# Kernel tuning notes

Measured on AMD Instinct MI355X. Metric: run time of the kernel, lower is better.

## Reference

```python
import jax, jax.numpy as jnp
import numpy as np

N_NODES = 50000
N_EDGES = 800000
IN_DIM = 128
HIDDEN = 16
HEADS1 = 8
OUT_DIM = 128
NEG_SLOPE = 0.2
EPS = 1e-16


def gat_conv(x, src, dst, W, att_src, att_dst, bias, heads, out_ch, concat, num_nodes):
    # x: [N, F_in]; W: [F_in, heads*out_ch]; att_*: [heads, out_ch]; bias: [heads*out_ch] or [out_ch]
    h = (x @ W).reshape(num_nodes, heads, out_ch)          # [N, H, C]
    a_src = jnp.einsum('nhc,hc->nh', h, att_src)           # [N, H]
    a_dst = jnp.einsum('nhc,hc->nh', h, att_dst)           # [N, H]
    alpha = a_src[src] + a_dst[dst]                        # [E, H]
    alpha = jax.nn.leaky_relu(alpha, NEG_SLOPE)
    # segment softmax over incoming edges of each dst node
    amax = jax.ops.segment_max(alpha, dst, num_segments=num_nodes)  # [N, H]
    e = jnp.exp(alpha - amax[dst])                         # [E, H]
    denom = jax.ops.segment_sum(e, dst, num_segments=num_nodes)     # [N, H]
    alpha = e / (denom[dst] + EPS)                         # [E, H]
    msg = h[src] * alpha[:, :, None]                       # [E, H, C]
    out = jax.ops.segment_sum(msg, dst, num_segments=num_nodes)     # [N, H, C]
    if concat:
        out = out.reshape(num_nodes, heads * out_ch)
    else:
        out = out.mean(axis=1)
    return out + bias


def setup_inputs() -> dict:
    key = jax.random.key(0)
    ks = jax.random.split(key, 12)
    x = jax.random.normal(ks[0], (N_NODES, IN_DIM), dtype=jnp.float32)
    edge_index = jax.random.randint(ks[1], (2, N_EDGES), 0, N_NODES, dtype=jnp.int32)
    s1 = 1.0 / np.sqrt(IN_DIM)
    s2 = 1.0 / np.sqrt(HIDDEN * HEADS1)
    W1 = jax.random.normal(ks[2], (IN_DIM, HEADS1 * HIDDEN), dtype=jnp.float32) * s1
    att_src1 = jax.random.normal(ks[3], (HEADS1, HIDDEN), dtype=jnp.float32) * s1
    att_dst1 = jax.random.normal(ks[4], (HEADS1, HIDDEN), dtype=jnp.float32) * s1
    bias1 = jnp.zeros((HEADS1 * HIDDEN,), dtype=jnp.float32)
    W2 = jax.random.normal(ks[5], (HEADS1 * HIDDEN, OUT_DIM), dtype=jnp.float32) * s2
    att_src2 = jax.random.normal(ks[6], (1, OUT_DIM), dtype=jnp.float32) * s2
    att_dst2 = jax.random.normal(ks[7], (1, OUT_DIM), dtype=jnp.float32) * s2
    bias2 = jnp.zeros((OUT_DIM,), dtype=jnp.float32)
    return {"x": x, "edge_index": edge_index,
            "W1": W1, "att_src1": att_src1, "att_dst1": att_dst1, "bias1": bias1,
            "W2": W2, "att_src2": att_src2, "att_dst2": att_dst2, "bias2": bias2}


def reference(x, edge_index, W1, att_src1, att_dst1, bias1, W2, att_src2, att_dst2, bias2):
    # eval mode: F.dropout and attention dropout are identity
    src, dst = edge_index[0], edge_index[1]
    h = gat_conv(x, src, dst, W1, att_src1, att_dst1, bias1,
                 HEADS1, HIDDEN, True, N_NODES)            # [N, HEADS1*HIDDEN]
    h = jax.nn.elu(h)
    out = gat_conv(h, src, dst, W2, att_src2, att_dst2, bias2,
                   1, OUT_DIM, False, N_NODES)             # [N, OUT_DIM]
    return out
```

## Files before the change

### kernel.cpp

```cpp
#include <hip/hip_runtime.h>

#define N_NODES 50000
#define N_EDGES 800000
#define CAP 64
#define NBUCK 196
#define NODES_PAD 50176
#define BBLK 256
#define EPB 3125
#define LOG2E 1.4426950408889634f

typedef unsigned int uint;
typedef unsigned short ushort;
typedef __attribute__((ext_vector_type(2))) float f32x2;
typedef __attribute__((ext_vector_type(4))) float f32x4;
typedef __attribute__((ext_vector_type(8))) short s16x8;

__device__ __forceinline__ f32x2 pk_add(f32x2 a, f32x2 b) {
    f32x2 d;
    asm("v_pk_add_f32 %0, %1, %2" : "=v"(d) : "v"(a), "v"(b));
    return d;
}
__device__ __forceinline__ f32x2 pk_mul(f32x2 a, f32x2 b) {
    f32x2 d;
    asm("v_pk_mul_f32 %0, %1, %2" : "=v"(d) : "v"(a), "v"(b));
    return d;
}
__device__ __forceinline__ f32x2 pk_fma(f32x2 a, f32x2 b, f32x2 c) {
    f32x2 d;
    asm("v_pk_fma_f32 %0, %1, %2, %3" : "=v"(d) : "v"(a), "v"(b), "v"(c));
    return d;
}

__device__ __forceinline__ ushort f2bf(float f) {
    uint u = __float_as_uint(f);
    u = (u + 0x7fffu + ((u >> 16) & 1u)) >> 16;
    return (ushort)u;
}
__device__ __forceinline__ float bf_lo(uint u) { return __uint_as_float(u << 16); }
__device__ __forceinline__ float bf_hi(uint u) { return __uint_as_float(u & 0xffff0000u); }

__global__ __launch_bounds__(256) void bin_count_kernel(
    const int* __restrict__ dstv, uint* __restrict__ counts)
{
    __shared__ uint hist[NBUCK];
    int tid = threadIdx.x, b = blockIdx.x;
    for (int k = tid; k < NBUCK; k += 256) hist[k] = 0;
    __syncthreads();
    int e0 = b * EPB;
    for (int i = tid; i < EPB; i += 256)
        atomicAdd(&hist[((uint)dstv[e0 + i]) >> 8], 1u);
    __syncthreads();
    for (int k = tid; k < NBUCK; k += 256) counts[k * BBLK + b] = hist[k];
}

__global__ __launch_bounds__(256) void scan1_kernel(
    const uint* __restrict__ counts, uint* __restrict__ ofs, uint* __restrict__ bsum)
{
    __shared__ uint wtot[4];
    int tid = threadIdx.x, k = blockIdx.x;
    int lane = tid & 63, wid = tid >> 6;
    uint v = counts[k * 256 + tid];
    uint inc = v;
    #pragma unroll
    for (int o = 1; o < 64; o <<= 1) {
        uint t = __shfl_up(inc, o);
        if (lane >= o) inc += t;
    }
    if (lane == 63) wtot[wid] = inc;
    __syncthreads();
    uint woff = 0;
    for (int w = 0; w < wid; w++) woff += wtot[w];
    uint excl = woff + inc - v;
    ofs[k * 256 + tid] = excl;
    if (tid == 255) bsum[k] = excl + v;
}

__global__ __launch_bounds__(64) void scan2_kernel(
    const uint* __restrict__ bsum, uint* __restrict__ bbase)
{
    int lane = threadIdx.x;
    int base = lane * 4;
    uint v[4];
    #pragma unroll
    for (int j = 0; j < 4; j++) v[j] = (base + j < NBUCK) ? bsum[base + j] : 0u;
    uint s = v[0] + v[1] + v[2] + v[3];
    uint inc = s;
    #pragma unroll
    for (int o = 1; o < 64; o <<= 1) {
        uint t = __shfl_up(inc, o);
        if (lane >= o) inc += t;
    }
    uint run = inc - s;
    #pragma unroll
    for (int j = 0; j < 4; j++) {
        if (base + j < NBUCK) { bbase[base + j] = run; run += v[j]; }
    }
}

__global__ __launch_bounds__(256) void bin_scatter_kernel(
    const int* __restrict__ srcv, const int* __restrict__ dstv,
    const uint* __restrict__ ofs, const uint* __restrict__ bbase,
    uint* __restrict__ binned)
{
    __shared__ uint cur[NBUCK];
    int tid = threadIdx.x, b = blockIdx.x;
    for (int k = tid; k < NBUCK; k += 256) cur[k] = ofs[k * BBLK + b] + bbase[k];
    __syncthreads();
    int e0 = b * EPB;
    for (int i = tid; i < EPB; i += 256) {
        int d = dstv[e0 + i], s = srcv[e0 + i];
        uint k = ((uint)d) >> 8;
        uint pos = atomicAdd(&cur[k], 1u);
        binned[pos] = (((uint)d & 255u) << 16) | (uint)s;
    }
}

__global__ __launch_bounds__(256) void build_kernel(
    const uint* __restrict__ binned, const uint* __restrict__ ofs,
    const uint* __restrict__ bbase,
    int* __restrict__ deg, ushort* __restrict__ list)
{
    __shared__ uint ldeg[256];
    __shared__ ushort llist[256 * CAP];
    int tid = threadIdx.x, k = blockIdx.x;
    ldeg[tid] = 0;
    __syncthreads();
    uint start = ofs[k * 256] + bbase[k];
    uint end = (k == NBUCK - 1) ? N_EDGES : (ofs[(k + 1) * 256] + bbase[k + 1]);
    for (uint i = start + tid; i < end; i += 256) {
        uint p = binned[i];
        uint nl = (p >> 16) & 255u;
        uint slot = atomicAdd(&ldeg[nl], 1u);
        if (slot < CAP) llist[(nl << 6) + slot] = (ushort)(p & 0xFFFFu);
    }
    __syncthreads();
    int node0 = k << 8;
    deg[node0 + tid] = (int)ldeg[tid];
    uint4* d4 = (uint4*)(list + (size_t)node0 * CAP);
    const uint4* s4 = (const uint4*)llist;
    for (int i = tid; i < 256 * CAP * 2 / 16; i += 256) d4[i] = s4[i];
}

__global__ __launch_bounds__(256) void prep_kernel(
    const float* __restrict__ W1, const float* __restrict__ as1, const float* __restrict__ ad1,
    const float* __restrict__ W2, const float* __restrict__ as2, const float* __restrict__ ad2,
    float* __restrict__ WS1, float* __restrict__ WS2)
{
    int idx = blockIdx.x * 256 + threadIdx.x;
    if (idx < 2048) {
        int k = idx >> 4, j = idx & 15;
        const float* att = (j < 8) ? as1 : ad1;
        int head = j & 7;
        float s = 0.f;
        #pragma unroll
        for (int c = 0; c < 16; c++)
            s += W1[k * 128 + head * 16 + c] * att[head * 16 + c];
        WS1[idx] = s * LOG2E;
    } else if (idx < 4096) {
        int idx2 = idx - 2048;
        int k = idx2 >> 4, j = idx2 & 15;
        float s = 0.f;
        if (j < 2) {
            const float* att = j ? ad2 : as2;
            for (int c = 0; c < 128; c++) s += W2[k * 128 + c] * att[c];
        }
        WS2[idx2] = s * LOG2E;
    }
}

template <int HEADS, bool ABF16>
__global__ __launch_bounds__(512) void gemm_mfma_kernel(
    const void* __restrict__ Av, const float* __restrict__ W,
    const float* __restrict__ WS,
    ushort* __restrict__ h16, float* __restrict__ a_src, float* __restrict__ a_dst,
    int nrows)
{
    __shared__ ushort Bf[2304 * 8];
    int tid = threadIdx.x;
    for (int idx = tid; idx < 2304; idx += 512) {
        int t = idx >> 8;
        int rem = idx & 255;
        int kt = rem >> 6, L = rem & 63;
        int col = L & 15;
        int kb = ((L >> 4) << 3) + (kt << 5);
        ushort tmp[8];
        if (t < 8) {
            #pragma unroll
            for (int j = 0; j < 8; j++)
                tmp[j] = f2bf(W[(size_t)(kb + j) * 128 + (t << 4) + col]);
        } else {
            #pragma unroll
            for (int j = 0; j < 8; j++)
                tmp[j] = f2bf(WS[(kb + j) * 16 + col]);
        }
        uint p0 = (uint)tmp[0] | ((uint)tmp[1] << 16);
        uint p1 = (uint)tmp[2] | ((uint)tmp[3] << 16);
        uint p2 = (uint)tmp[4] | ((uint)tmp[5] << 16);
        uint p3 = (uint)tmp[6] | ((uint)tmp[7] << 16);
        *(uint4*)&Bf[idx * 8] = make_uint4(p0, p1, p2, p3);
    }
    __syncthreads();

    int lane = tid & 63;
    int wv = tid >> 6;
    int row0 = (blockIdx.x * 8 + wv) * 16;
    if (row0 >= nrows) return;

    int m = lane & 15, kg = lane >> 4;
    s16x8 afrag[4];
    if (ABF16) {
        const ushort* arow = (const ushort*)Av + (size_t)(row0 + m) * 128 + (kg << 3);
        #pragma unroll
        for (int kt = 0; kt < 4; kt++)
            afrag[kt] = *(const s16x8*)(arow + (kt << 5));
    } else {
        const float* arow = (const float*)Av + (size_t)(row0 + m) * 128 + (kg << 3);
        #pragma unroll
        for (int kt = 0; kt < 4; kt++) {
            float4 f0 = *(const float4*)(arow + (kt << 5));
            float4 f1 = *(const float4*)(arow + (kt << 5) + 4);
            union { s16x8 v; ushort us[8]; } uu;
            uu.us[0] = f2bf(f0.x); uu.us[1] = f2bf(f0.y);
            uu.us[2] = f2bf(f0.z); uu.us[3] = f2bf(f0.w);
            uu.us[4] = f2bf(f1.x); uu.us[5] = f2bf(f1.y);
            uu.us[6] = f2bf(f1.z); uu.us[7] = f2bf(f1.w);
            afrag[kt] = uu.v;
        }
    }

    f32x4 acc[9];
    #pragma unroll
    for (int t = 0; t < 9; t++) acc[t] = (f32x4){0.f, 0.f, 0.f, 0.f};
    #pragma unroll
    for (int t = 0; t < 9; t++) {
        #pragma unroll
        for (int kt = 0; kt < 4; kt++) {
            s16x8 b = *(const s16x8*)&Bf[(((t << 2) + kt) * 64 + lane) * 8];
            acc[t] = __builtin_amdgcn_mfma_f32_16x16x32_bf16(afrag[kt], b, acc[t], 0, 0, 0);
        }
    }

    int colw = lane & 15;
    int rbase = row0 + ((lane >> 4) << 2);
    #pragma unroll
    for (int t = 0; t < 8; t++) {
        #pragma unroll
        for (int r = 0; r < 4; r++)
            h16[(size_t)(rbase + r) * 128 + (t << 4) + colw] = f2bf(acc[t][r]);
    }
    #pragma unroll
    for (int r = 0; r < 4; r++) {
        float v = acc[8][r];
        int row = rbase + r;
        if (HEADS == 8) {
            if (colw < 8) a_src[row * 8 + colw] = v;
            else          a_dst[row * 8 + (colw - 8)] = v;
        } else {
            if (colw == 0)      a_src[row] = v;
            else if (colw == 1) a_dst[row] = v;
        }
    }
}

template <int HEADS, bool ELU, bool OUT16>
__global__ __launch_bounds__(256) void agg_kernel(
    const ushort* __restrict__ h16, const ushort* __restrict__ list,
    const int* __restrict__ deg,
    const float* __restrict__ a_src, const float* __restrict__ a_dst,
    const float* __restrict__ bias, void* __restrict__ outv)
{
    __shared__ float w_lds[4][HEADS][65];
    __shared__ int s_lds[4][64];
    __shared__ float sh_l[4][8];
    int lane = threadIdx.x & 63;
    int wv = threadIdx.x >> 6;
    int n = blockIdx.x * 4 + wv;
    int d = min(deg[n], CAP);
    bool valid = lane < d;
    int s = valid ? (int)list[n * CAP + lane] : 0;
    s_lds[wv][lane] = s << 8;

    if (HEADS == 8) {
        float4 u0 = *(const float4*)&a_src[s * 8];
        float4 u1 = *(const float4*)&a_src[s * 8 + 4];
        float4 v0 = *(const float4*)&a_dst[n * 8];
        float4 v1 = *(const float4*)&a_dst[n * 8 + 4];
        float al[8] = {u0.x + v0.x, u0.y + v0.y, u0.z + v0.z, u0.w + v0.w,
                       u1.x + v1.x, u1.y + v1.y, u1.z + v1.z, u1.w + v1.w};
        float eh[8];
        #pragma unroll
        for (int hh = 0; hh < 8; hh++) {
            float a = fmaxf(al[hh], 0.2f * al[hh]);
            eh[hh] = valid ? exp2f(a) : 0.f;
            w_lds[wv][hh][lane] = eh[hh];
        }
        f32x2 s01 = {eh[0], eh[1]}, s23 = {eh[2], eh[3]};
        f32x2 s45 = {eh[4], eh[5]}, s67 = {eh[6], eh[7]};
        auto lvl = [&](int mm) {
            f32x2 t;
            t.x = __shfl_xor(s01.x, mm); t.y = __shfl_xor(s01.y, mm); s01 = pk_add(s01, t);
            t.x = __shfl_xor(s23.x, mm); t.y = __shfl_xor(s23.y, mm); s23 = pk_add(s23, t);
            t.x = __shfl_xor(s45.x, mm); t.y = __shfl_xor(s45.y, mm); s45 = pk_add(s45, t);
            t.x = __shfl_xor(s67.x, mm); t.y = __shfl_xor(s67.y, mm); s67 = pk_add(s67, t);
        };
        lvl(1); lvl(2); lvl(4); lvl(8);
        if (d > 16) lvl(16);
        if (d > 32) lvl(32);
        if (lane == 0) {
            *(f32x2*)&sh_l[wv][0] = s01; *(f32x2*)&sh_l[wv][2] = s23;
            *(f32x2*)&sh_l[wv][4] = s45; *(f32x2*)&sh_l[wv][6] = s67;
        }
    } else {
        float a = a_src[s] + a_dst[n];
        a = fmaxf(a, 0.2f * a);
        float eh0 = valid ? exp2f(a) : 0.f;
        w_lds[wv][0][lane] = eh0;
        float sh = eh0;
        sh += __shfl_xor(sh, 1); sh += __shfl_xor(sh, 2);
        sh += __shfl_xor(sh, 4); sh += __shfl_xor(sh, 8);
        if (d > 16) sh += __shfl_xor(sh, 16);
        if (d > 32) sh += __shfl_xor(sh, 32);
        if (lane == 0) sh_l[wv][0] = sh;
    }

    int half = lane >> 5;
    int lq = lane & 31;
    int c0 = lq << 2;
    int g = (HEADS == 8) ? (lq >> 2) : 0;
    const char* hp = (const char*)h16 + (c0 << 1);
    f32x2 acc01 = {0.f, 0.f}, acc23 = {0.f, 0.f};
    int d8 = (d + 7) & ~7;
    for (int e0 = 0; e0 < d8; e0 += 8) {
        int soff[4]; float wv4[4]; uint2 u[4];
        #pragma unroll
        for (int r = 0; r < 4; r++) {
            int e = e0 + (r << 1) + half;
            soff[r] = s_lds[wv][e];
            wv4[r] = w_lds[wv][g][e];
        }
        #pragma unroll
        for (int r = 0; r < 4; r++)
            u[r] = *(const uint2*)(hp + soff[r]);
        #pragma unroll
        for (int r = 0; r < 4; r++) {
            f32x2 wp = {wv4[r], wv4[r]};
            f32x2 lo = {bf_lo(u[r].x), bf_hi(u[r].x)};
            f32x2 hi = {bf_lo(u[r].y), bf_hi(u[r].y)};
            acc01 = pk_fma(wp, lo, acc01);
            acc23 = pk_fma(wp, hi, acc23);
        }
    }
    f32x2 t;
    t.x = __shfl_xor(acc01.x, 32); t.y = __shfl_xor(acc01.y, 32); acc01 = pk_add(acc01, t);
    t.x = __shfl_xor(acc23.x, 32); t.y = __shfl_xor(acc23.y, 32); acc23 = pk_add(acc23, t);

    float shv = sh_l[wv][g];
    float r = __builtin_amdgcn_rcpf(shv + 1e-16f);
    f32x2 rr = {r, r};
    acc01 = pk_mul(acc01, rr);
    acc23 = pk_mul(acc23, rr);
    float4 bv = *(const float4*)&bias[c0];
    float o0 = acc01.x + bv.x, o1 = acc01.y + bv.y;
    float o2 = acc23.x + bv.z, o3 = acc23.y + bv.w;
    if (ELU) {
        o0 = o0 > 0.f ? o0 : __expf(o0) - 1.f;
        o1 = o1 > 0.f ? o1 : __expf(o1) - 1.f;
        o2 = o2 > 0.f ? o2 : __expf(o2) - 1.f;
        o3 = o3 > 0.f ? o3 : __expf(o3) - 1.f;
    }
    if (lane < 32) {
        if (OUT16) {
            uint2 pk;
            pk.x = (uint)f2bf(o0) | ((uint)f2bf(o1) << 16);
            pk.y = (uint)f2bf(o2) | ((uint)f2bf(o3) << 16);
            *(uint2*)((ushort*)outv + (size_t)n * 128 + c0) = pk;
        } else {
            *(float4*)((float*)outv + (size_t)n * 128 + c0) = make_float4(o0, o1, o2, o3);
        }
    }
}

extern "C" void kernel_launch(void* const* d_in, const int* in_sizes, int n_in,
                              void* d_out, int out_size, void* d_ws, size_t ws_size,
                              hipStream_t stream)
{
    (void)in_sizes; (void)n_in; (void)out_size; (void)ws_size;
    const float* x   = (const float*)d_in[0];
    const int*   ei  = (const int*)d_in[1];
    const float* W1  = (const float*)d_in[2];
    const float* as1 = (const float*)d_in[3];
    const float* ad1 = (const float*)d_in[4];
    const float* b1  = (const float*)d_in[5];
    const float* W2  = (const float*)d_in[6];
    const float* as2 = (const float*)d_in[7];
    const float* ad2 = (const float*)d_in[8];
    const float* b2  = (const float*)d_in[9];
    float* out = (float*)d_out;
    const int* srcv = ei;
    const int* dstv = ei + N_EDGES;

    char* ws = (char*)d_ws;
    size_t off = 0;
    auto alloc = [&](size_t bytes) {
        void* p = ws + off;
        off += (bytes + 255) & ~(size_t)255;
        return p;
    };
    ushort* h1_16 = (ushort*)alloc((size_t)N_NODES * 128 * 2);
    ushort* h2_16 = (ushort*)alloc((size_t)N_NODES * 128 * 2);
    ushort* h1b   = (ushort*)alloc((size_t)N_NODES * 128 * 2);
    float*  asrc1 = (float*)alloc((size_t)N_NODES * 8 * 4);
    float*  adst1 = (float*)alloc((size_t)N_NODES * 8 * 4);
    float*  asrc2 = (float*)alloc((size_t)N_NODES * 4);
    float*  adst2 = (float*)alloc((size_t)N_NODES * 4);
    int*    degp  = (int*)alloc((size_t)NODES_PAD * 4);
    ushort* list  = (ushort*)alloc((size_t)NODES_PAD * CAP * 2);
    float*  WS1   = (float*)alloc(128 * 16 * 4);
    float*  WS2   = (float*)alloc(128 * 16 * 4);
    uint* binned = (uint*)h1b;
    uint* counts = binned + N_EDGES;
    uint* ofsp   = counts + NODES_PAD;
    uint* bsum   = ofsp + NODES_PAD;
    uint* bbase  = bsum + NBUCK;

    const int NG = (N_NODES + 3) / 4;
    const int GB = (N_NODES / 16 + 7) / 8;

    prep_kernel<<<16, 256, 0, stream>>>(W1, as1, ad1, W2, as2, ad2, WS1, WS2);
    bin_count_kernel<<<BBLK, 256, 0, stream>>>(dstv, counts);
    scan1_kernel<<<NBUCK, 256, 0, stream>>>(counts, ofsp, bsum);
    scan2_kernel<<<1, 64, 0, stream>>>(bsum, bbase);
    bin_scatter_kernel<<<BBLK, 256, 0, stream>>>(srcv, dstv, ofsp, bbase, binned);
    build_kernel<<<NBUCK, 256, 0, stream>>>(binned, ofsp, bbase, degp, list);

    gemm_mfma_kernel<8, false><<<GB, 512, 0, stream>>>(x, W1, WS1, h1_16, asrc1, adst1, N_NODES);
    agg_kernel<8, true, true><<<NG, 256, 0, stream>>>(h1_16, list, degp, asrc1, adst1, b1, h1b);

    gemm_mfma_kernel<1, true><<<GB, 512, 0, stream>>>(h1b, W2, WS2, h2_16, asrc2, adst2, N_NODES);
    agg_kernel<1, false, false><<<NG, 256, 0, stream>>>(h2_16, list, degp, asrc2, adst2, b2, out);
}
```

Baseline: 125.5 us.

## Software-pipeline neighbor feature gathers with double-buffered 16-edge chunks

Result: no change. 124.7 us (-0.7%).

```diff
diff --git a/kernel.cpp b/kernel.cpp
--- a/kernel.cpp
+++ b/kernel.cpp
@@ -280,11 +280,49 @@
     int s = valid ? (int)list[n * CAP + lane] : 0;
     s_lds[wv][lane] = s << 8;
 
+    float4 u0, u1, v0, v1;
+    float a1s = 0.f, a1d = 0.f;
     if (HEADS == 8) {
-        float4 u0 = *(const float4*)&a_src[s * 8];
-        float4 u1 = *(const float4*)&a_src[s * 8 + 4];
-        float4 v0 = *(const float4*)&a_dst[n * 8];
-        float4 v1 = *(const float4*)&a_dst[n * 8 + 4];
+        u0 = *(const float4*)&a_src[s * 8];
+        u1 = *(const float4*)&a_src[s * 8 + 4];
+        v0 = *(const float4*)&a_dst[n * 8];
+        v1 = *(const float4*)&a_dst[n * 8 + 4];
+    } else {
+        a1s = a_src[s]; a1d = a_dst[n];
+    }
+
+    int half = lane >> 5;
+    int lq = lane & 31;
+    int c0 = lq << 2;
+    int g = (HEADS == 8) ? (lq >> 2) : 0;
+    const char* hp = (const char*)h16 + (c0 << 1);
+    int d16 = (d + 15) & ~15;
+
+    uint2 uA[8], uB[8];
+    auto issue = [&](uint2 (&u)[8], int base) {
+        #pragma unroll
+        for (int r = 0; r < 8; r++) {
+            int e = base + (r << 1) + half;
+            u[r] = *(const uint2*)(hp + s_lds[wv][e]);
+        }
+    };
+    f32x2 acc01 = {0.f, 0.f}, acc23 = {0.f, 0.f};
+    auto fmachunk = [&](uint2 (&u)[8], int base) {
+        #pragma unroll
+        for (int r = 0; r < 8; r++) {
+            int e = base + (r << 1) + half;
+            float w = w_lds[wv][g][e];
+            f32x2 wp = {w, w};
+            f32x2 lo = {bf_lo(u[r].x), bf_hi(u[r].x)};
+            f32x2 hi = {bf_lo(u[r].y), bf_hi(u[r].y)};
+            acc01 = pk_fma(wp, lo, acc01);
+            acc23 = pk_fma(wp, hi, acc23);
+        }
+    };
+
+    if (d16 > 0) issue(uA, 0);
+
+    if (HEADS == 8) {
         float al[8] = {u0.x + v0.x, u0.y + v0.y, u0.z + v0.z, u0.w + v0.w,
                        u1.x + v1.x, u1.y + v1.y, u1.z + v1.z, u1.w + v1.w};
         float eh[8];
@@ -311,7 +349,7 @@
             *(f32x2*)&sh_l[wv][4] = s45; *(f32x2*)&sh_l[wv][6] = s67;
         }
     } else {
-        float a = a_src[s] + a_dst[n];
+        float a = a1s + a1d;
         a = fmaxf(a, 0.2f * a);
         float eh0 = valid ? exp2f(a) : 0.f;
         w_lds[wv][0][lane] = eh0;
@@ -323,33 +361,14 @@
         if (lane == 0) sh_l[wv][0] = sh;
     }
 
-    int half = lane >> 5;
-    int lq = lane & 31;
-    int c0 = lq << 2;
-    int g = (HEADS == 8) ? (lq >> 2) : 0;
-    const char* hp = (const char*)h16 + (c0 << 1);
-    f32x2 acc01 = {0.f, 0.f}, acc23 = {0.f, 0.f};
-    int d8 = (d + 7) & ~7;
-    for (int e0 = 0; e0 < d8; e0 += 8) {
-        int soff[4]; float wv4[4]; uint2 u[4];
-        #pragma unroll
-        for (int r = 0; r < 4; r++) {
-            int e = e0 + (r << 1) + half;
-            soff[r] = s_lds[wv][e];
-            wv4[r] = w_lds[wv][g][e];
-        }
-        #pragma unroll
-        for (int r = 0; r < 4; r++)
-            u[r] = *(const uint2*)(hp + soff[r]);
-        #pragma unroll
-        for (int r = 0; r < 4; r++) {
-            f32x2 wp = {wv4[r], wv4[r]};
-            f32x2 lo = {bf_lo(u[r].x), bf_hi(u[r].x)};
-            f32x2 hi = {bf_lo(u[r].y), bf_hi(u[r].y)};
-            acc01 = pk_fma(wp, lo, acc01);
-            acc23 = pk_fma(wp, hi, acc23);
-        }
-    }
+    if (d16 > 16) issue(uB, 16);
+    if (d16 > 0)  fmachunk(uA, 0);
+    if (d16 > 32) issue(uA, 32);
+    if (d16 > 16) fmachunk(uB, 16);
+    if (d16 > 48) issue(uB, 48);
+    if (d16 > 32) fmachunk(uA, 32);
+    if (d16 > 48) fmachunk(uB, 48);
+
     f32x2 t;
     t.x = __shfl_xor(acc01.x, 32); t.y = __shfl_xor(acc01.y, 32); acc01 = pk_add(acc01, t);
     t.x = __shfl_xor(acc23.x, 32); t.y = __shfl_xor(acc23.y, 32); acc23 = pk_add(acc23, t);
```

## Shrink graph-build buckets to 64 nodes and fuse weight prep into scan kernel

Applied to the files above, without the earlier changes.

New measurement: 124.1 us. About the same (-1.2%).

```diff
diff --git a/kernel.cpp b/kernel.cpp
--- a/kernel.cpp
+++ b/kernel.cpp
@@ -3,8 +3,8 @@
 #define N_NODES 50000
 #define N_EDGES 800000
 #define CAP 64
-#define NBUCK 196
-#define NODES_PAD 50176
+#define NBUCK 782
+#define NODES_PAD 50048
 #define BBLK 256
 #define EPB 3125
 #define LOG2E 1.4426950408889634f
@@ -48,7 +48,7 @@
     __syncthreads();
     int e0 = b * EPB;
     for (int i = tid; i < EPB; i += 256)
-        atomicAdd(&hist[((uint)dstv[e0 + i]) >> 8], 1u);
+        atomicAdd(&hist[((uint)dstv[e0 + i]) >> 6], 1u);
     __syncthreads();
     for (int k = tid; k < NBUCK; k += 256) counts[k * BBLK + b] = hist[k];
 }
@@ -75,25 +75,58 @@
     if (tid == 255) bsum[k] = excl + v;
 }
 
-__global__ __launch_bounds__(64) void scan2_kernel(
-    const uint* __restrict__ bsum, uint* __restrict__ bbase)
-{
-    int lane = threadIdx.x;
-    int base = lane * 4;
-    uint v[4];
-    #pragma unroll
-    for (int j = 0; j < 4; j++) v[j] = (base + j < NBUCK) ? bsum[base + j] : 0u;
-    uint s = v[0] + v[1] + v[2] + v[3];
-    uint inc = s;
-    #pragma unroll
-    for (int o = 1; o < 64; o <<= 1) {
-        uint t = __shfl_up(inc, o);
-        if (lane >= o) inc += t;
-    }
-    uint run = inc - s;
-    #pragma unroll
-    for (int j = 0; j < 4; j++) {
-        if (base + j < NBUCK) { bbase[base + j] = run; run += v[j]; }
+__global__ __launch_bounds__(256) void scan2_prep_kernel(
+    const uint* __restrict__ bsum, uint* __restrict__ bbase,
+    const float* __restrict__ W1, const float* __restrict__ as1, const float* __restrict__ ad1,
+    const float* __restrict__ W2, const float* __restrict__ as2, const float* __restrict__ ad2,
+    float* __restrict__ WS1, float* __restrict__ WS2)
+{
+    int bid = blockIdx.x;
+    int tid = threadIdx.x;
+    if (bid == 0) {
+        __shared__ uint wtot[4];
+        int lane = tid & 63, wid = tid >> 6;
+        int base = tid * 4;
+        uint v[4];
+        #pragma unroll
+        for (int j = 0; j < 4; j++) v[j] = (base + j < NBUCK) ? bsum[base + j] : 0u;
+        uint s = v[0] + v[1] + v[2] + v[3];
+        uint inc = s;
+        #pragma unroll
+        for (int o = 1; o < 64; o <<= 1) {
+            uint t = __shfl_up(inc, o);
+            if (lane >= o) inc += t;
+        }
+        if (lane == 63) wtot[wid] = inc;
+        __syncthreads();
+        uint woff = 0;
+        for (int w = 0; w < wid; w++) woff += wtot[w];
+        uint run = woff + inc - s;
+        #pragma unroll
+        for (int j = 0; j < 4; j++) {
+            if (base + j < NBUCK) { bbase[base + j] = run; run += v[j]; }
+        }
+    } else {
+        int idx = (bid - 1) * 256 + tid;
+        if (idx < 2048) {
+            int k = idx >> 4, j = idx & 15;
+            const float* att = (j < 8) ? as1 : ad1;
+            int head = j & 7;
+            float s = 0.f;
+            #pragma unroll
+            for (int c = 0; c < 16; c++)
+                s += W1[k * 128 + head * 16 + c] * att[head * 16 + c];
+            WS1[idx] = s * LOG2E;
+        } else {
+            int idx2 = idx - 2048;
+            int k = idx2 >> 4, j = idx2 & 15;
+            float s = 0.f;
+            if (j < 2) {
+                const float* att = j ? ad2 : as2;
+                for (int c = 0; c < 128; c++) s += W2[k * 128 + c] * att[c];
+            }
+            WS2[idx2] = s * LOG2E;
+        }
     }
 }
 
@@ -109,9 +142,9 @@
     int e0 = b * EPB;
     for (int i = tid; i < EPB; i += 256) {
         int d = dstv[e0 + i], s = srcv[e0 + i];
-        uint k = ((uint)d) >> 8;
+        uint k = ((uint)d) >> 6;
         uint pos = atomicAdd(&cur[k], 1u);
-        binned[pos] = (((uint)d & 255u) << 16) | (uint)s;
+        binned[pos] = (((uint)d & 63u) << 16) | (uint)s;
     }
 }
 
@@ -120,52 +153,26 @@
     const uint* __restrict__ bbase,
     int* __restrict__ deg, ushort* __restrict__ list)
 {
-    __shared__ uint ldeg[256];
-    __shared__ ushort llist[256 * CAP];
+    __shared__ uint ldeg[64];
+    __shared__ ushort llist[64 * CAP];
     int tid = threadIdx.x, k = blockIdx.x;
-    ldeg[tid] = 0;
+    if (tid < 64) ldeg[tid] = 0;
+    for (int i = tid; i < 64 * CAP / 2; i += 256) ((uint*)llist)[i] = 0;
     __syncthreads();
     uint start = ofs[k * 256] + bbase[k];
     uint end = (k == NBUCK - 1) ? N_EDGES : (ofs[(k + 1) * 256] + bbase[k + 1]);
     for (uint i = start + tid; i < end; i += 256) {
         uint p = binned[i];
-        uint nl = (p >> 16) & 255u;
+        uint nl = (p >> 16) & 63u;
         uint slot = atomicAdd(&ldeg[nl], 1u);
         if (slot < CAP) llist[(nl << 6) + slot] = (ushort)(p & 0xFFFFu);
     }
     __syncthreads();
-    int node0 = k << 8;
-    deg[node0 + tid] = (int)ldeg[tid];
+    int node0 = k << 6;
+    if (tid < 64) deg[node0 + tid] = (int)ldeg[tid];
     uint4* d4 = (uint4*)(list + (size_t)node0 * CAP);
     const uint4* s4 = (const uint4*)llist;
-    for (int i = tid; i < 256 * CAP * 2 / 16; i += 256) d4[i] = s4[i];
-}
-
-__global__ __launch_bounds__(256) void prep_kernel(
-    const float* __restrict__ W1, const float* __restrict__ as1, const float* __restrict__ ad1,
-    const float* __restrict__ W2, const float* __restrict__ as2, const float* __restrict__ ad2,
-    float* __restrict__ WS1, float* __restrict__ WS2)
-{
-    int idx = blockIdx.x * 256 + threadIdx.x;
-    if (idx < 2048) {
-        int k = idx >> 4, j = idx & 15;
-        const float* att = (j < 8) ? as1 : ad1;
-        int head = j & 7;
-        float s = 0.f;
-        #pragma unroll
-        for (int c = 0; c < 16; c++)
-            s += W1[k * 128 + head * 16 + c] * att[head * 16 + c];
-        WS1[idx] = s * LOG2E;
-    } else if (idx < 4096) {
-        int idx2 = idx - 2048;
-        int k = idx2 >> 4, j = idx2 & 15;
-        float s = 0.f;
-        if (j < 2) {
-            const float* att = j ? ad2 : as2;
-            for (int c = 0; c < 128; c++) s += W2[k * 128 + c] * att[c];
-        }
-        WS2[idx2] = s * LOG2E;
-    }
+    for (int i = tid; i < 64 * CAP * 2 / 16; i += 256) d4[i] = s4[i];
 }
 
 template <int HEADS, bool ABF16>
@@ -419,17 +426,16 @@
     float*  WS2   = (float*)alloc(128 * 16 * 4);
     uint* binned = (uint*)h1b;
     uint* counts = binned + N_EDGES;
-    uint* ofsp   = counts + NODES_PAD;
-    uint* bsum   = ofsp + NODES_PAD;
+    uint* ofsp   = counts + NBUCK * BBLK;
+    uint* bsum   = ofsp + NBUCK * BBLK;
     uint* bbase  = bsum + NBUCK;
 
     const int NG = (N_NODES + 3) / 4;
     const int GB = (N_NODES / 16 + 7) / 8;
 
-    prep_kernel<<<16, 256, 0, stream>>>(W1, as1, ad1, W2, as2, ad2, WS1, WS2);
     bin_count_kernel<<<BBLK, 256, 0, stream>>>(dstv, counts);
     scan1_kernel<<<NBUCK, 256, 0, stream>>>(counts, ofsp, bsum);
-    scan2_kernel<<<1, 64, 0, stream>>>(bsum, bbase);
+    scan2_prep_kernel<<<17, 256, 0, stream>>>(bsum, bbase, W1, as1, ad1, W2, as2, ad2, WS1, WS2);
     bin_scatter_kernel<<<BBLK, 256, 0, stream>>>(srcv, dstv, ofsp, bbase, binned);
     build_kernel<<<NBUCK, 256, 0, stream>>>(binned, ofsp, bbase, degp, list);
 
```
